# Kernel tuning notes

Measured on AMD Instinct MI355X. Metric: run time of the kernel, lower is better.

## Reference

```python
import jax, jax.numpy as jnp
import numpy as np

N, E, DIN, DOUT, EDIM = 100000, 1000000, 64, 64, 64


def _xavier(k, shape, gain=1.0):
    fan_out, fan_in = shape
    a = gain * np.sqrt(6.0 / (fan_in + fan_out))
    return jax.random.uniform(k, shape, jnp.float32, -a, a)


def setup_inputs() -> dict:
    key = jax.random.key(0)
    ks = jax.random.split(key, 16)
    relu_gain = float(np.sqrt(2.0))  # nn.init.calculate_gain('relu')
    return {
        "nfeats": jax.random.normal(ks[0], (N, DIN), jnp.float32),
        "efeats": jax.random.normal(ks[1], (E, EDIM), jnp.float32),
        "src": jax.random.randint(ks[2], (E,), 0, N),
        "dst": jax.random.randint(ks[3], (E,), 0, N),
        "e_perm": jax.random.permutation(ks[4], E),
        # layer 0 params (torch Linear layout: [out, in])
        "Wmsg0": _xavier(ks[5], (DOUT, DIN + EDIM)),
        "bmsg0": jnp.zeros((DOUT,), jnp.float32),
        "Wapply0": _xavier(ks[6], (DOUT, DIN + DOUT), relu_gain),
        "bapply0": jnp.zeros((DOUT,), jnp.float32),
        # layer 1 params
        "Wmsg1": _xavier(ks[7], (DOUT, DOUT + EDIM)),
        "bmsg1": jnp.zeros((DOUT,), jnp.float32),
        "Wapply1": _xavier(ks[8], (DOUT, DOUT + DOUT), relu_gain),
        "bapply1": jnp.zeros((DOUT,), jnp.float32),
    }


def _sage_layer(h, ef, src, dst, Wmsg, bmsg, Wap, bap, n_nodes):
    # message: W_msg(cat(src_h, e_h)) per edge  -> [E, dout]
    m = jnp.concatenate([h[src], ef], axis=1) @ Wmsg.T + bmsg
    # mean-reduce messages onto destination nodes
    s = jax.ops.segment_sum(m, dst, num_segments=n_nodes)
    cnt = jax.ops.segment_sum(jnp.ones((dst.shape[0],), m.dtype), dst, num_segments=n_nodes)
    h_neigh = s / jnp.maximum(cnt, 1.0)[:, None]  # zero-in-degree nodes -> 0
    return jax.nn.relu(jnp.concatenate([h, h_neigh], axis=1) @ Wap.T + bap)


def _bce_with_logits(x, target):
    # mean(log(1+exp(x)) - x*target), numerically stable via logaddexp
    return jnp.mean(jnp.logaddexp(0.0, x) - x * target)


def reference(nfeats, efeats, src, dst, e_perm,
              Wmsg0, bmsg0, Wapply0, bapply0,
              Wmsg1, bmsg1, Wapply1, bapply1):
    n_nodes = nfeats.shape[0]

    def encode(ef):
        h = _sage_layer(nfeats, ef, src, dst, Wmsg0, bmsg0, Wapply0, bapply0, n_nodes)
        h = _sage_layer(h, ef, src, dst, Wmsg1, bmsg1, Wapply1, bapply1, n_nodes)
        return h

    positive = encode(efeats)
    negative = encode(efeats[e_perm])  # corrupted view: permuted edge features
    P_LABEL, N_LABEL = 1.0, 0.0  # DGI p / n targets
    return _bce_with_logits(positive, P_LABEL) + _bce_with_logits(negative, N_LABEL)
```

## Files before the change

### kernel.cpp

```cpp
#include <hip/hip_runtime.h>
#include <math.h>

#define NN 100000
#define NE 1000000
#define D  64
#define NB_SCAN 391


__global__ __launch_bounds__(256) void k_hist(
    const int* __restrict__ dst, int* __restrict__ counts, int* __restrict__ rank)
{
    int e = blockIdx.x * 256 + threadIdx.x;
    if (e >= NE) return;
    rank[e] = atomicAdd(&counts[dst[e]], 1);
}

__global__ __launch_bounds__(256) void k_scan1(
    const int* __restrict__ counts, int* __restrict__ row_start, int* __restrict__ bsum)
{
    __shared__ int s[256];
    int t = threadIdx.x;
    int i = blockIdx.x * 256 + t;
    int v = (i < NN) ? counts[i] : 0;
    s[t] = v; __syncthreads();
#pragma unroll
    for (int off = 1; off < 256; off <<= 1) {
        int add = (t >= off) ? s[t - off] : 0;
        __syncthreads();
        s[t] += add;
        __syncthreads();
    }
    if (i < NN) row_start[i] = s[t] - v;
    if (t == 255) bsum[blockIdx.x] = s[255];
}

__global__ __launch_bounds__(512) void k_scan2(
    const int* __restrict__ bsum, int* __restrict__ boff, int* __restrict__ row_start)
{
    __shared__ int s[512];
    int t = threadIdx.x;
    int v = (t < NB_SCAN) ? bsum[t] : 0;
    s[t] = v; __syncthreads();
#pragma unroll
    for (int off = 1; off < 512; off <<= 1) {
        int add = (t >= off) ? s[t - off] : 0;
        __syncthreads();
        s[t] += add;
        __syncthreads();
    }
    if (t < NB_SCAN) boff[t] = s[t] - v;
    if (t == 0) row_start[NN] = NE;
}

__global__ __launch_bounds__(256) void k_scan3(
    int* __restrict__ row_start, const int* __restrict__ boff)
{
    int i = blockIdx.x * 256 + threadIdx.x;
    if (i < NN) row_start[i] += boff[i >> 8];
}

__global__ __launch_bounds__(256) void k_scatter(
    const int* __restrict__ dst, const int* __restrict__ src,
    const int* __restrict__ perm, const int* __restrict__ rank,
    const int* __restrict__ row_start, int4* __restrict__ sorted,
    int* __restrict__ srcS)
{
    int e = blockIdx.x * 256 + threadIdx.x;
    if (e >= NE) return;
    int s = src[e];
    int pos = row_start[dst[e]] + rank[e];
    sorted[pos] = make_int4(s, e, perm[e], 0);
    srcS[pos] = s;
}


__global__ __launch_bounds__(256) void pull_pass1(
    const int4* __restrict__ sorted, const int* __restrict__ row_start,
    const float* __restrict__ nfeats, const float* __restrict__ efeats,
    float* __restrict__ hsum0, float* __restrict__ efsP, float* __restrict__ efsN)
{
    int gt = blockIdx.x * 256 + threadIdx.x;
    int w = gt >> 6, lane = gt & 63;
    if (w >= NN) return;
    int es = lane >> 4, c4 = (lane & 15) << 2;
    int beg = row_start[w], end = row_start[w + 1];

    float an0 = 0.f, an1 = 0.f, an2 = 0.f, an3 = 0.f;
    float ap0 = 0.f, ap1 = 0.f, ap2 = 0.f, ap3 = 0.f;
    float ag0 = 0.f, ag1 = 0.f, ag2 = 0.f, ag3 = 0.f;
    int i = beg + es;
    int4 q = (i < end) ? sorted[i] : make_int4(0, 0, 0, 0);
#pragma unroll 1
    for (; i < end; i += 4) {
        int inext = i + 4;
        int4 qn = (inext < end) ? sorted[inext] : make_int4(0, 0, 0, 0);
        float4 n  = *(const float4*)(nfeats + (size_t)q.x * D + c4);
        float4 ep = *(const float4*)(efeats + (size_t)q.y * D + c4);
        float4 en = *(const float4*)(efeats + (size_t)q.z * D + c4);
        an0 += n.x;  an1 += n.y;  an2 += n.z;  an3 += n.w;
        ap0 += ep.x; ap1 += ep.y; ap2 += ep.z; ap3 += ep.w;
        ag0 += en.x; ag1 += en.y; ag2 += en.z; ag3 += en.w;
        q = qn;
    }
#pragma unroll
    for (int off = 16; off <= 32; off <<= 1) {
        an0 += __shfl_xor(an0, off, 64); an1 += __shfl_xor(an1, off, 64);
        an2 += __shfl_xor(an2, off, 64); an3 += __shfl_xor(an3, off, 64);
        ap0 += __shfl_xor(ap0, off, 64); ap1 += __shfl_xor(ap1, off, 64);
        ap2 += __shfl_xor(ap2, off, 64); ap3 += __shfl_xor(ap3, off, 64);
        ag0 += __shfl_xor(ag0, off, 64); ag1 += __shfl_xor(ag1, off, 64);
        ag2 += __shfl_xor(ag2, off, 64); ag3 += __shfl_xor(ag3, off, 64);
    }
    if (lane < 16) {
        *(float4*)(hsum0 + (size_t)w * D + c4) = make_float4(an0, an1, an2, an3);
        *(float4*)(efsP  + (size_t)w * D + c4) = make_float4(ap0, ap1, ap2, ap3);
        *(float4*)(efsN  + (size_t)w * D + c4) = make_float4(ag0, ag1, ag2, ag3);
    }
}

__global__ __launch_bounds__(256) void pull_h2(
    const int* __restrict__ srcS, const int* __restrict__ row_start,
    const float* __restrict__ hP, const float* __restrict__ hN,
    float* __restrict__ hsumP, float* __restrict__ hsumN)
{
    int gt = blockIdx.x * 256 + threadIdx.x;
    int w = gt >> 6, lane = gt & 63;
    if (w >= NN) return;
    int es = lane >> 4, c4 = (lane & 15) << 2;
    int beg = row_start[w], end = row_start[w + 1];

    float p0 = 0.f, p1 = 0.f, p2 = 0.f, p3 = 0.f;
    float n0 = 0.f, n1 = 0.f, n2 = 0.f, n3 = 0.f;
    int i = beg + es;
    int s = (i < end) ? srcS[i] : 0;
#pragma unroll 1
    for (; i < end; i += 4) {
        int inext = i + 4;
        int sn = (inext < end) ? srcS[inext] : 0;
        float4 vP = *(const float4*)(hP + (size_t)s * D + c4);
        float4 vN = *(const float4*)(hN + (size_t)s * D + c4);
        p0 += vP.x; p1 += vP.y; p2 += vP.z; p3 += vP.w;
        n0 += vN.x; n1 += vN.y; n2 += vN.z; n3 += vN.w;
        s = sn;
    }
#pragma unroll
    for (int off = 16; off <= 32; off <<= 1) {
        p0 += __shfl_xor(p0, off, 64); p1 += __shfl_xor(p1, off, 64);
        p2 += __shfl_xor(p2, off, 64); p3 += __shfl_xor(p3, off, 64);
        n0 += __shfl_xor(n0, off, 64); n1 += __shfl_xor(n1, off, 64);
        n2 += __shfl_xor(n2, off, 64); n3 += __shfl_xor(n3, off, 64);
    }
    if (lane < 16) {
        *(float4*)(hsumP + (size_t)w * D + c4) = make_float4(p0, p1, p2, p3);
        *(float4*)(hsumN + (size_t)w * D + c4) = make_float4(n0, n1, n2, n3);
    }
}

__global__ __launch_bounds__(256, 4) void fused_layer(
    const float* __restrict__ Hsum, const float* __restrict__ Esum,
    const float* __restrict__ Hprev, const int* __restrict__ counts,
    const float* __restrict__ Wmsg, const float* __restrict__ bmsg,
    const float* __restrict__ Wap, const float* __restrict__ bap,
    float* __restrict__ Hout, int do_loss, int is_neg, float* __restrict__ loss_out)
{
    __shared__ __align__(16) float As[64][68];
    __shared__ __align__(16) float Bs[128][68];
    int tid = threadIdx.x;
    int block0 = blockIdx.x * 64;
    int tx = tid & 15, ty = tid >> 4;
    int tx4 = tx << 2;

#pragma unroll 1
    for (int i = 0; i < 32; ++i) {
        int idx = i * 256 + tid;
        Bs[idx & 127][idx >> 7] = Wmsg[idx];
    }

    float acc[4][4] = {};
#pragma unroll
    for (int half = 0; half < 2; ++half) {
        const float* Asrc = half ? Esum : Hsum;
        __syncthreads();
#pragma unroll
        for (int g = 0; g < 4; ++g) {
            int idx = g * 256 + tid;
            int node = idx >> 4, c = (idx & 15) << 2;
            int gn = block0 + node;
            float4 v = make_float4(0.f, 0.f, 0.f, 0.f);
            if (gn < NN) v = *(const float4*)(Asrc + (size_t)gn * D + c);
            *(float4*)&As[node][c] = v;
        }
        __syncthreads();
        int hb = half * 64;
#pragma unroll 1
        for (int k0 = 0; k0 < 64; k0 += 4) {
            float a[4][4];
#pragma unroll
            for (int i = 0; i < 4; ++i)
                *(float4*)&a[i][0] = *(const float4*)&As[ty + 16 * i][k0];
#pragma unroll
            for (int kk = 0; kk < 4; ++kk) {
                float4 b = *(const float4*)&Bs[hb + k0 + kk][tx4];
#pragma unroll
                for (int i = 0; i < 4; ++i) {
                    acc[i][0] += a[i][kk] * b.x;
                    acc[i][1] += a[i][kk] * b.y;
                    acc[i][2] += a[i][kk] * b.z;
                    acc[i][3] += a[i][kk] * b.w;
                }
            }
        }
    }

    float bm[4];
#pragma unroll
    for (int j = 0; j < 4; ++j) bm[j] = bmsg[tx4 + j];
    float msg[4][4];
#pragma unroll
    for (int i = 0; i < 4; ++i) {
        int gn = block0 + ty + 16 * i;
        float c = (gn < NN) ? (float)counts[gn] : 0.f;
        float inv = 1.0f / fmaxf(c, 1.0f);
#pragma unroll
        for (int j = 0; j < 4; ++j) msg[i][j] = (acc[i][j] + c * bm[j]) * inv;
    }

    __syncthreads();
#pragma unroll 1
    for (int i = 0; i < 32; ++i) {
        int idx = i * 256 + tid;
        Bs[idx & 127][idx >> 7] = Wap[idx];
    }
#pragma unroll
    for (int i = 0; i < 4; ++i)
        *(float4*)&As[ty + 16 * i][tx4] = make_float4(msg[i][0], msg[i][1], msg[i][2], msg[i][3]);
    __syncthreads();

    float acc2[4][4] = {};
#pragma unroll 1
    for (int k0 = 0; k0 < 64; k0 += 4) {
        float a[4][4];
#pragma unroll
        for (int i = 0; i < 4; ++i)
            *(float4*)&a[i][0] = *(const float4*)&As[ty + 16 * i][k0];
#pragma unroll
        for (int kk = 0; kk < 4; ++kk) {
            float4 b = *(const float4*)&Bs[64 + k0 + kk][tx4];
#pragma unroll
            for (int i = 0; i < 4; ++i) {
                acc2[i][0] += a[i][kk] * b.x;
                acc2[i][1] += a[i][kk] * b.y;
                acc2[i][2] += a[i][kk] * b.z;
                acc2[i][3] += a[i][kk] * b.w;
            }
        }
    }
    __syncthreads();
#pragma unroll
    for (int g = 0; g < 4; ++g) {
        int idx = g * 256 + tid;
        int node = idx >> 4, c = (idx & 15) << 2;
        int gn = block0 + node;
        float4 v = make_float4(0.f, 0.f, 0.f, 0.f);
        if (gn < NN) v = *(const float4*)(Hprev + (size_t)gn * D + c);
        *(float4*)&As[node][c] = v;
    }
    __syncthreads();
#pragma unroll 1
    for (int k0 = 0; k0 < 64; k0 += 4) {
        float a[4][4];
#pragma unroll
        for (int i = 0; i < 4; ++i)
            *(float4*)&a[i][0] = *(const float4*)&As[ty + 16 * i][k0];
#pragma unroll
        for (int kk = 0; kk < 4; ++kk) {
            float4 b = *(const float4*)&Bs[k0 + kk][tx4];
#pragma unroll
            for (int i = 0; i < 4; ++i) {
                acc2[i][0] += a[i][kk] * b.x;
                acc2[i][1] += a[i][kk] * b.y;
                acc2[i][2] += a[i][kk] * b.z;
                acc2[i][3] += a[i][kk] * b.w;
            }
        }
    }

    float ba[4];
#pragma unroll
    for (int j = 0; j < 4; ++j) ba[j] = bap[tx4 + j];
    if (!do_loss) {
#pragma unroll
        for (int i = 0; i < 4; ++i) {
            int gn = block0 + ty + 16 * i;
            if (gn >= NN) continue;
#pragma unroll
            for (int j = 0; j < 4; ++j)
                Hout[(size_t)gn * D + tx4 + j] = fmaxf(acc2[i][j] + ba[j], 0.f);
        }
    } else {
        float lsum = 0.f;
#pragma unroll
        for (int i = 0; i < 4; ++i) {
            int gn = block0 + ty + 16 * i;
            if (gn >= NN) continue;
#pragma unroll
            for (int j = 0; j < 4; ++j) {
                float x = fmaxf(acc2[i][j] + ba[j], 0.f);
                float l = log1pf(expf(-x));
                if (is_neg) l += x;
                lsum += l;
            }
        }
#pragma unroll
        for (int off = 32; off; off >>= 1) lsum += __shfl_down(lsum, off, 64);
        if ((tid & 63) == 0)
            unsafeAtomicAdd(loss_out, lsum * (1.0f / 6400000.0f));
    }
}

extern "C" void kernel_launch(void* const* d_in, const int* in_sizes, int n_in,
                              void* d_out, int out_size, void* d_ws, size_t ws_size,
                              hipStream_t stream) {
    (void)in_sizes; (void)n_in; (void)out_size; (void)ws_size;
    const float* nfeats = (const float*)d_in[0];
    const float* efeats = (const float*)d_in[1];
    const int*   src    = (const int*)d_in[2];
    const int*   dst    = (const int*)d_in[3];
    const int*   perm   = (const int*)d_in[4];
    const float* Wmsg0  = (const float*)d_in[5];
    const float* bmsg0  = (const float*)d_in[6];
    const float* Wap0   = (const float*)d_in[7];
    const float* bap0   = (const float*)d_in[8];
    const float* Wmsg1  = (const float*)d_in[9];
    const float* bmsg1  = (const float*)d_in[10];
    const float* Wap1   = (const float*)d_in[11];
    const float* bap1   = (const float*)d_in[12];
    float* out = (float*)d_out;

    const size_t NV = (size_t)NN * D;
    char* p = (char*)d_ws;
    int4* sorted   = (int4*)p;               p += (size_t)NE * 16;
    int*  srcS     = (int*)p;                p += (size_t)NE * 4;
    int*  rank     = (int*)p;                p += (size_t)NE * 4;
    int*  counts   = (int*)p;                p += ((NN + 15) & ~15) * 4;
    int*  rowst    = (int*)p;                p += ((NN + 16) & ~15) * 4;
    int*  bsum     = (int*)p;                p += 512 * 4;
    int*  boff     = (int*)p;                p += 512 * 4;
    float* efsP    = (float*)p;              p += NV * 4;
    float* efsN    = (float*)p;              p += NV * 4;
    float* hsum0   = (float*)p;              p += NV * 4;
    float* h1P     = (float*)p;              p += NV * 4;
    float* h1N     = (float*)p;              p += NV * 4;
    float* hsum1P  = (float*)p;              p += NV * 4;
    float* hsum1N  = (float*)p;              p += NV * 4;

    const int EGb = (NE + 255) / 256;
    const int PGb = ((size_t)NN * 64 + 255) / 256;
    const int NG  = (NN + 63) / 64;

    hipMemsetAsync(counts, 0, (size_t)NN * 4, stream);
    hipMemsetAsync(d_out, 0, 4, stream);

    k_hist<<<EGb, 256, 0, stream>>>(dst, counts, rank);
    k_scan1<<<NB_SCAN, 256, 0, stream>>>(counts, rowst, bsum);
    k_scan2<<<1, 512, 0, stream>>>(bsum, boff, rowst);
    k_scan3<<<NB_SCAN, 256, 0, stream>>>(rowst, boff);
    k_scatter<<<EGb, 256, 0, stream>>>(dst, src, perm, rank, rowst, sorted, srcS);

    pull_pass1<<<PGb, 256, 0, stream>>>(sorted, rowst, nfeats, efeats, hsum0, efsP, efsN);

    fused_layer<<<NG, 256, 0, stream>>>(hsum0, efsP, nfeats, counts,
                                        Wmsg0, bmsg0, Wap0, bap0, h1P, 0, 0, nullptr);
    fused_layer<<<NG, 256, 0, stream>>>(hsum0, efsN, nfeats, counts,
                                        Wmsg0, bmsg0, Wap0, bap0, h1N, 0, 0, nullptr);

    pull_h2<<<PGb, 256, 0, stream>>>(srcS, rowst, h1P, h1N, hsum1P, hsum1N);

    fused_layer<<<NG, 256, 0, stream>>>(hsum1P, efsP, h1P, counts,
                                        Wmsg1, bmsg1, Wap1, bap1, nullptr, 1, 0, out);
    fused_layer<<<NG, 256, 0, stream>>>(hsum1N, efsN, h1N, counts,
                                        Wmsg1, bmsg1, Wap1, bap1, nullptr, 1, 1, out);
}
```

Measured before the change: 1.041 ms.

## Fuse positive/negative dense layers into single kernels and drop srcS array

The four per-view dense layer launches are merged into two kernels that process both the positive and negative views per node tile. In layer 0 the shared Hsum·Wmsg and Hprev·Wap partial products are computed once and reused for both views, and weight staging is amortized. The separate srcS array is removed: pull_h2 reads the src index from the int4 sorted array instead, which saves a scatter write stream but makes the second gather read 16-byte records instead of 4-byte ones. The change also adds register pressure from holding two message tiles per thread.

```diff
diff --git a/kernel.cpp b/kernel.cpp
--- a/kernel.cpp
+++ b/kernel.cpp
@@ -62,15 +62,12 @@
 __global__ __launch_bounds__(256) void k_scatter(
     const int* __restrict__ dst, const int* __restrict__ src,
     const int* __restrict__ perm, const int* __restrict__ rank,
-    const int* __restrict__ row_start, int4* __restrict__ sorted,
-    int* __restrict__ srcS)
+    const int* __restrict__ row_start, int4* __restrict__ sorted)
 {
     int e = blockIdx.x * 256 + threadIdx.x;
     if (e >= NE) return;
-    int s = src[e];
     int pos = row_start[dst[e]] + rank[e];
-    sorted[pos] = make_int4(s, e, perm[e], 0);
-    srcS[pos] = s;
+    sorted[pos] = make_int4(src[e], e, perm[e], 0);
 }
 
 
@@ -119,7 +116,7 @@
 }
 
 __global__ __launch_bounds__(256) void pull_h2(
-    const int* __restrict__ srcS, const int* __restrict__ row_start,
+    const int4* __restrict__ sorted, const int* __restrict__ row_start,
     const float* __restrict__ hP, const float* __restrict__ hN,
     float* __restrict__ hsumP, float* __restrict__ hsumN)
 {
@@ -132,11 +129,11 @@
     float p0 = 0.f, p1 = 0.f, p2 = 0.f, p3 = 0.f;
     float n0 = 0.f, n1 = 0.f, n2 = 0.f, n3 = 0.f;
     int i = beg + es;
-    int s = (i < end) ? srcS[i] : 0;
+    int s = (i < end) ? sorted[i].x : 0;
 #pragma unroll 1
     for (; i < end; i += 4) {
         int inext = i + 4;
-        int sn = (inext < end) ? srcS[inext] : 0;
+        int sn = (inext < end) ? sorted[inext].x : 0;
         float4 vP = *(const float4*)(hP + (size_t)s * D + c4);
         float4 vN = *(const float4*)(hN + (size_t)s * D + c4);
         p0 += vP.x; p1 += vP.y; p2 += vP.z; p3 += vP.w;
@@ -156,12 +153,59 @@
     }
 }
 
-__global__ __launch_bounds__(256, 4) void fused_layer(
-    const float* __restrict__ Hsum, const float* __restrict__ Esum,
-    const float* __restrict__ Hprev, const int* __restrict__ counts,
+
+__device__ __forceinline__ void gemm_half(
+    float acc[4][4], const float (*As)[68], const float (*Bs)[68],
+    int ty, int tx4, int hb)
+{
+#pragma unroll 1
+    for (int k0 = 0; k0 < 64; k0 += 4) {
+        float a[4][4];
+#pragma unroll
+        for (int i = 0; i < 4; ++i)
+            *(float4*)&a[i][0] = *(const float4*)&As[ty + 16 * i][k0];
+#pragma unroll
+        for (int kk = 0; kk < 4; ++kk) {
+            float4 b = *(const float4*)&Bs[hb + k0 + kk][tx4];
+#pragma unroll
+            for (int i = 0; i < 4; ++i) {
+                acc[i][0] += a[i][kk] * b.x;
+                acc[i][1] += a[i][kk] * b.y;
+                acc[i][2] += a[i][kk] * b.z;
+                acc[i][3] += a[i][kk] * b.w;
+            }
+        }
+    }
+}
+
+#define STAGE_A(SRC) { \
+    _Pragma("unroll") \
+    for (int g = 0; g < 4; ++g) { \
+        int idx = g * 256 + tid; \
+        int node = idx >> 4, c = (idx & 15) << 2; \
+        int gn = block0 + node; \
+        float4 v = make_float4(0.f, 0.f, 0.f, 0.f); \
+        if (gn < NN) v = *(const float4*)((SRC) + (size_t)gn * D + c); \
+        *(float4*)&As[node][c] = v; } }
+
+#define STAGE_B(W) { \
+    _Pragma("unroll 1") \
+    for (int i = 0; i < 32; ++i) { \
+        int idx = i * 256 + tid; \
+        Bs[idx & 127][idx >> 7] = (W)[idx]; } }
+
+#define STORE_MSG(M) { \
+    _Pragma("unroll") \
+    for (int i = 0; i < 4; ++i) \
+        *(float4*)&As[ty + 16 * i][tx4] = make_float4((M)[i][0], (M)[i][1], (M)[i][2], (M)[i][3]); }
+
+__global__ __launch_bounds__(256, 4) void fused2_l0(
+    const float* __restrict__ Hsum, const float* __restrict__ EsumP,
+    const float* __restrict__ EsumN, const float* __restrict__ Hprev,
+    const int* __restrict__ counts,
     const float* __restrict__ Wmsg, const float* __restrict__ bmsg,
     const float* __restrict__ Wap, const float* __restrict__ bap,
-    float* __restrict__ Hout, int do_loss, int is_neg, float* __restrict__ loss_out)
+    float* __restrict__ HoutP, float* __restrict__ HoutN)
 {
     __shared__ __align__(16) float As[64][68];
     __shared__ __align__(16) float Bs[128][68];
@@ -170,152 +214,169 @@
     int tx = tid & 15, ty = tid >> 4;
     int tx4 = tx << 2;
 
-#pragma unroll 1
-    for (int i = 0; i < 32; ++i) {
-        int idx = i * 256 + tid;
-        Bs[idx & 127][idx >> 7] = Wmsg[idx];
-    }
-
-    float acc[4][4] = {};
-#pragma unroll
-    for (int half = 0; half < 2; ++half) {
-        const float* Asrc = half ? Esum : Hsum;
-        __syncthreads();
-#pragma unroll
-        for (int g = 0; g < 4; ++g) {
-            int idx = g * 256 + tid;
-            int node = idx >> 4, c = (idx & 15) << 2;
-            int gn = block0 + node;
-            float4 v = make_float4(0.f, 0.f, 0.f, 0.f);
-            if (gn < NN) v = *(const float4*)(Asrc + (size_t)gn * D + c);
-            *(float4*)&As[node][c] = v;
-        }
-        __syncthreads();
-        int hb = half * 64;
-#pragma unroll 1
-        for (int k0 = 0; k0 < 64; k0 += 4) {
-            float a[4][4];
-#pragma unroll
-            for (int i = 0; i < 4; ++i)
-                *(float4*)&a[i][0] = *(const float4*)&As[ty + 16 * i][k0];
-#pragma unroll
-            for (int kk = 0; kk < 4; ++kk) {
-                float4 b = *(const float4*)&Bs[hb + k0 + kk][tx4];
-#pragma unroll
-                for (int i = 0; i < 4; ++i) {
-                    acc[i][0] += a[i][kk] * b.x;
-                    acc[i][1] += a[i][kk] * b.y;
-                    acc[i][2] += a[i][kk] * b.z;
-                    acc[i][3] += a[i][kk] * b.w;
-                }
-            }
-        }
-    }
-
-    float bm[4];
-#pragma unroll
-    for (int j = 0; j < 4; ++j) bm[j] = bmsg[tx4 + j];
-    float msg[4][4];
+    float cnt[4], inv[4];
 #pragma unroll
     for (int i = 0; i < 4; ++i) {
         int gn = block0 + ty + 16 * i;
-        float c = (gn < NN) ? (float)counts[gn] : 0.f;
-        float inv = 1.0f / fmaxf(c, 1.0f);
-#pragma unroll
-        for (int j = 0; j < 4; ++j) msg[i][j] = (acc[i][j] + c * bm[j]) * inv;
-    }
-
-    __syncthreads();
+        cnt[i] = (gn < NN) ? (float)counts[gn] : 0.f;
+        inv[i] = 1.0f / fmaxf(cnt[i], 1.0f);
+    }
+    float bm[4], ba[4];
+#pragma unroll
+    for (int j = 0; j < 4; ++j) { bm[j] = bmsg[tx4 + j]; ba[j] = bap[tx4 + j]; }
+
+    STAGE_B(Wmsg);
+    STAGE_A(Hsum);
+    __syncthreads();
+    float accb[4][4] = {};
+    gemm_half(accb, As, Bs, ty, tx4, 0);
+    __syncthreads();
+    STAGE_A(EsumP);
+    __syncthreads();
+    float msgP[4][4];
+#pragma unroll
+    for (int i = 0; i < 4; ++i)
+#pragma unroll
+        for (int j = 0; j < 4; ++j) msgP[i][j] = accb[i][j];
+    gemm_half(msgP, As, Bs, ty, tx4, 64);
+#pragma unroll
+    for (int i = 0; i < 4; ++i)
+#pragma unroll
+        for (int j = 0; j < 4; ++j) msgP[i][j] = (msgP[i][j] + cnt[i] * bm[j]) * inv[i];
+    __syncthreads();
+    STAGE_A(EsumN);
+    __syncthreads();
+    gemm_half(accb, As, Bs, ty, tx4, 64);
+    float msgN[4][4];
+#pragma unroll
+    for (int i = 0; i < 4; ++i)
+#pragma unroll
+        for (int j = 0; j < 4; ++j) msgN[i][j] = (accb[i][j] + cnt[i] * bm[j]) * inv[i];
+
+    __syncthreads();
+    STAGE_B(Wap);
+    STAGE_A(Hprev);
+    __syncthreads();
+    float acc2b[4][4] = {};
+    gemm_half(acc2b, As, Bs, ty, tx4, 0);
+
+    __syncthreads();
+    STORE_MSG(msgP);
+    __syncthreads();
+    float acc2[4][4];
+#pragma unroll
+    for (int i = 0; i < 4; ++i)
+#pragma unroll
+        for (int j = 0; j < 4; ++j) acc2[i][j] = acc2b[i][j];
+    gemm_half(acc2, As, Bs, ty, tx4, 64);
+#pragma unroll
+    for (int i = 0; i < 4; ++i) {
+        int gn = block0 + ty + 16 * i;
+        if (gn >= NN) continue;
+#pragma unroll
+        for (int j = 0; j < 4; ++j)
+            HoutP[(size_t)gn * D + tx4 + j] = fmaxf(acc2[i][j] + ba[j], 0.f);
+    }
+
+    __syncthreads();
+    STORE_MSG(msgN);
+    __syncthreads();
+#pragma unroll
+    for (int i = 0; i < 4; ++i)
+#pragma unroll
+        for (int j = 0; j < 4; ++j) acc2[i][j] = acc2b[i][j];
+    gemm_half(acc2, As, Bs, ty, tx4, 64);
+#pragma unroll
+    for (int i = 0; i < 4; ++i) {
+        int gn = block0 + ty + 16 * i;
+        if (gn >= NN) continue;
+#pragma unroll
+        for (int j = 0; j < 4; ++j)
+            HoutN[(size_t)gn * D + tx4 + j] = fmaxf(acc2[i][j] + ba[j], 0.f);
+    }
+}
+
+__global__ __launch_bounds__(256, 4) void fused2_l1loss(
+    const float* __restrict__ HsumP, const float* __restrict__ HsumN,
+    const float* __restrict__ EsumP, const float* __restrict__ EsumN,
+    const float* __restrict__ HprevP, const float* __restrict__ HprevN,
+    const int* __restrict__ counts,
+    const float* __restrict__ Wmsg, const float* __restrict__ bmsg,
+    const float* __restrict__ Wap, const float* __restrict__ bap,
+    float* __restrict__ loss_out)
+{
+    __shared__ __align__(16) float As[64][68];
+    __shared__ __align__(16) float Bs[128][68];
+    int tid = threadIdx.x;
+    int block0 = blockIdx.x * 64;
+    int tx = tid & 15, ty = tid >> 4;
+    int tx4 = tx << 2;
+
+    float cnt[4], inv[4];
+#pragma unroll
+    for (int i = 0; i < 4; ++i) {
+        int gn = block0 + ty + 16 * i;
+        cnt[i] = (gn < NN) ? (float)counts[gn] : 0.f;
+        inv[i] = 1.0f / fmaxf(cnt[i], 1.0f);
+    }
+    float bm[4], ba[4];
+#pragma unroll
+    for (int j = 0; j < 4; ++j) { bm[j] = bmsg[tx4 + j]; ba[j] = bap[tx4 + j]; }
+
+    float lsum = 0.f;
 #pragma unroll 1
-    for (int i = 0; i < 32; ++i) {
-        int idx = i * 256 + tid;
-        Bs[idx & 127][idx >> 7] = Wap[idx];
-    }
-#pragma unroll
-    for (int i = 0; i < 4; ++i)
-        *(float4*)&As[ty + 16 * i][tx4] = make_float4(msg[i][0], msg[i][1], msg[i][2], msg[i][3]);
-    __syncthreads();
-
-    float acc2[4][4] = {};
-#pragma unroll 1
-    for (int k0 = 0; k0 < 64; k0 += 4) {
-        float a[4][4];
+    for (int side = 0; side < 2; ++side) {
+        const float* Hsum  = side ? HsumN  : HsumP;
+        const float* Esum  = side ? EsumN  : EsumP;
+        const float* Hprev = side ? HprevN : HprevP;
+
+        if (side == 0) { STAGE_B(Wmsg); }
+        else {
+            __syncthreads();
+            STAGE_B(Wmsg);
+        }
+        STAGE_A(Hsum);
+        __syncthreads();
+        float acc[4][4] = {};
+        gemm_half(acc, As, Bs, ty, tx4, 0);
+        __syncthreads();
+        STAGE_A(Esum);
+        __syncthreads();
+        gemm_half(acc, As, Bs, ty, tx4, 64);
+        float msg[4][4];
 #pragma unroll
         for (int i = 0; i < 4; ++i)
-            *(float4*)&a[i][0] = *(const float4*)&As[ty + 16 * i][k0];
-#pragma unroll
-        for (int kk = 0; kk < 4; ++kk) {
-            float4 b = *(const float4*)&Bs[64 + k0 + kk][tx4];
-#pragma unroll
-            for (int i = 0; i < 4; ++i) {
-                acc2[i][0] += a[i][kk] * b.x;
-                acc2[i][1] += a[i][kk] * b.y;
-                acc2[i][2] += a[i][kk] * b.z;
-                acc2[i][3] += a[i][kk] * b.w;
-            }
-        }
-    }
-    __syncthreads();
-#pragma unroll
-    for (int g = 0; g < 4; ++g) {
-        int idx = g * 256 + tid;
-        int node = idx >> 4, c = (idx & 15) << 2;
-        int gn = block0 + node;
-        float4 v = make_float4(0.f, 0.f, 0.f, 0.f);
-        if (gn < NN) v = *(const float4*)(Hprev + (size_t)gn * D + c);
-        *(float4*)&As[node][c] = v;
-    }
-    __syncthreads();
-#pragma unroll 1
-    for (int k0 = 0; k0 < 64; k0 += 4) {
-        float a[4][4];
-#pragma unroll
-        for (int i = 0; i < 4; ++i)
-            *(float4*)&a[i][0] = *(const float4*)&As[ty + 16 * i][k0];
-#pragma unroll
-        for (int kk = 0; kk < 4; ++kk) {
-            float4 b = *(const float4*)&Bs[k0 + kk][tx4];
-#pragma unroll
-            for (int i = 0; i < 4; ++i) {
-                acc2[i][0] += a[i][kk] * b.x;
-                acc2[i][1] += a[i][kk] * b.y;
-                acc2[i][2] += a[i][kk] * b.z;
-                acc2[i][3] += a[i][kk] * b.w;
-            }
-        }
-    }
-
-    float ba[4];
-#pragma unroll
-    for (int j = 0; j < 4; ++j) ba[j] = bap[tx4 + j];
-    if (!do_loss) {
+#pragma unroll
+            for (int j = 0; j < 4; ++j) msg[i][j] = (acc[i][j] + cnt[i] * bm[j]) * inv[i];
+
+        __syncthreads();
+        STAGE_B(Wap);
+        STAGE_A(Hprev);
+        __syncthreads();
+        float acc2[4][4] = {};
+        gemm_half(acc2, As, Bs, ty, tx4, 0);
+        __syncthreads();
+        STORE_MSG(msg);
+        __syncthreads();
+        gemm_half(acc2, As, Bs, ty, tx4, 64);
+
 #pragma unroll
         for (int i = 0; i < 4; ++i) {
             int gn = block0 + ty + 16 * i;
             if (gn >= NN) continue;
 #pragma unroll
-            for (int j = 0; j < 4; ++j)
-                Hout[(size_t)gn * D + tx4 + j] = fmaxf(acc2[i][j] + ba[j], 0.f);
-        }
-    } else {
-        float lsum = 0.f;
-#pragma unroll
-        for (int i = 0; i < 4; ++i) {
-            int gn = block0 + ty + 16 * i;
-            if (gn >= NN) continue;
-#pragma unroll
             for (int j = 0; j < 4; ++j) {
                 float x = fmaxf(acc2[i][j] + ba[j], 0.f);
                 float l = log1pf(expf(-x));
-                if (is_neg) l += x;
+                if (side) l += x;
                 lsum += l;
             }
         }
-#pragma unroll
-        for (int off = 32; off; off >>= 1) lsum += __shfl_down(lsum, off, 64);
-        if ((tid & 63) == 0)
-            unsafeAtomicAdd(loss_out, lsum * (1.0f / 6400000.0f));
-    }
+    }
+#pragma unroll
+    for (int off = 32; off; off >>= 1) lsum += __shfl_down(lsum, off, 64);
+    if ((tid & 63) == 0)
+        unsafeAtomicAdd(loss_out, lsum * (1.0f / 6400000.0f));
 }
 
 extern "C" void kernel_launch(void* const* d_in, const int* in_sizes, int n_in,
@@ -340,7 +401,6 @@
     const size_t NV = (size_t)NN * D;
     char* p = (char*)d_ws;
     int4* sorted   = (int4*)p;               p += (size_t)NE * 16;
-    int*  srcS     = (int*)p;                p += (size_t)NE * 4;
     int*  rank     = (int*)p;                p += (size_t)NE * 4;
     int*  counts   = (int*)p;                p += ((NN + 15) & ~15) * 4;
     int*  rowst    = (int*)p;                p += ((NN + 16) & ~15) * 4;
@@ -365,19 +425,15 @@
     k_scan1<<<NB_SCAN, 256, 0, stream>>>(counts, rowst, bsum);
     k_scan2<<<1, 512, 0, stream>>>(bsum, boff, rowst);
     k_scan3<<<NB_SCAN, 256, 0, stream>>>(rowst, boff);
-    k_scatter<<<EGb, 256, 0, stream>>>(dst, src, perm, rank, rowst, sorted, srcS);
+    k_scatter<<<EGb, 256, 0, stream>>>(dst, src, perm, rank, rowst, sorted);
 
     pull_pass1<<<PGb, 256, 0, stream>>>(sorted, rowst, nfeats, efeats, hsum0, efsP, efsN);
 
-    fused_layer<<<NG, 256, 0, stream>>>(hsum0, efsP, nfeats, counts,
-                                        Wmsg0, bmsg0, Wap0, bap0, h1P, 0, 0, nullptr);
-    fused_layer<<<NG, 256, 0, stream>>>(hsum0, efsN, nfeats, counts,
-                                        Wmsg0, bmsg0, Wap0, bap0, h1N, 0, 0, nullptr);
-
-    pull_h2<<<PGb, 256, 0, stream>>>(srcS, rowst, h1P, h1N, hsum1P, hsum1N);
-
-    fused_layer<<<NG, 256, 0, stream>>>(hsum1P, efsP, h1P, counts,
-                                        Wmsg1, bmsg1, Wap1, bap1, nullptr, 1, 0, out);
-    fused_layer<<<NG, 256, 0, stream>>>(hsum1N, efsN, h1N, counts,
-                                        Wmsg1, bmsg1, Wap1, bap1, nullptr, 1, 1, out);
-}
+    fused2_l0<<<NG, 256, 0, stream>>>(hsum0, efsP, efsN, nfeats, counts,
+                                      Wmsg0, bmsg0, Wap0, bap0, h1P, h1N);
+
+    pull_h2<<<PGb, 256, 0, stream>>>(sorted, rowst, h1P, h1N, hsum1P, hsum1N);
+
+    fused2_l1loss<<<NG, 256, 0, stream>>>(hsum1P, hsum1N, efsP, efsN, h1P, h1N,
+                                          counts, Wmsg1, bmsg1, Wap1, bap1, out);
+}
```

Result: faster. 911.6 us (-12.4%).
